# Kernel optimization log

Hardware: AMD Instinct MI355X
Metric: run time of the kernel (lower is better)

Reference implementation:

```python
import jax, jax.numpy as jnp
import numpy as np
from jax import lax

K = 10  # k_neighbors (k = min(k, N); N=1024 so k=10)


def setup_inputs() -> dict:
    key = jax.random.key(0)
    ks = jax.random.split(key, 6)
    B, N, M, D = 4, 1024, 8, 128
    PROJ, NC, OUT = 64, 10, 128
    x = jax.random.normal(ks[0], (B, N, M, D), dtype=jnp.float32)
    # Linear params (torch stores weight as [out, in])
    W_proj_w = jax.random.normal(ks[1], (PROJ, D), dtype=jnp.float32) / np.sqrt(D)
    W_proj_b = jnp.zeros((PROJ,), dtype=jnp.float32)
    C = jax.random.normal(ks[2], (NC, PROJ), dtype=jnp.float32) * np.sqrt(2.0 / (NC + PROJ))
    Theta_w = jax.random.normal(ks[3], (OUT, D), dtype=jnp.float32) / np.sqrt(D)
    Theta_b = jnp.zeros((OUT,), dtype=jnp.float32)
    return {"x": x, "W_proj_w": W_proj_w, "W_proj_b": W_proj_b, "C": C,
            "Theta_w": Theta_w, "Theta_b": Theta_b}


def _forward(x, W_proj_w, W_proj_b, C, Theta_w, Theta_b):
    B, N, M, D = x.shape
    BM = B * M
    x_flat = jnp.transpose(x, (0, 2, 1, 3)).reshape(BM, N, D)
    Z = x_flat @ W_proj_w.T + W_proj_b  # [BM, N, P]
    # squared euclidean pairwise distances (same topk ordering as cdist)
    sq = jnp.sum(Z * Z, axis=-1)  # [BM, N]
    d2 = sq[:, :, None] + sq[:, None, :] - 2.0 * jnp.einsum('bnp,bmp->bnm', Z, Z)
    _, idx = lax.top_k(-d2, K)  # k smallest distances -> [BM, N, K]
    # scatter 1.0 at neighbor indices
    b_ix = jnp.arange(BM)[:, None, None]
    r_ix = jnp.arange(N)[None, :, None]
    H_knn = jnp.zeros((BM, N, N), dtype=jnp.float32).at[b_ix, r_ix, idx].set(1.0)
    H_cluster = jax.nn.softmax(Z @ C.T, axis=-1)  # [BM, N, NC]
    H = jnp.concatenate([H_knn, H_cluster], axis=-1)  # [BM, N, N+NC]
    # hypergraph conv with degree normalization
    D_e = H.sum(axis=1)  # [BM, E]
    D_e_inv = jnp.where(D_e > 0, 1.0 / jnp.maximum(D_e, 1e-12), 0.0)
    D_v = H.sum(axis=2)  # [BM, N]
    D_v_inv_sqrt = jnp.where(D_v > 0, 1.0 / jnp.sqrt(jnp.maximum(D_v, 1e-12)), 0.0)
    X_trans = x_flat @ Theta_w.T + Theta_b  # [BM, N, F]
    out = D_v_inv_sqrt[:, :, None] * X_trans
    out = jnp.einsum('bne,bnf->bef', H, out)   # H^T @ out
    out = D_e_inv[:, :, None] * out
    out = jnp.einsum('bne,bef->bnf', H, out)   # H @ out
    out = D_v_inv_sqrt[:, :, None] * out
    out = jax.nn.elu(out)
    return jnp.transpose(out.reshape(B, M, N, -1), (0, 2, 1, 3))  # [B, N, M, F]


def reference(x, W_proj_w, W_proj_b, C, Theta_w, Theta_b):
    return _forward(x, W_proj_w, W_proj_b, C, Theta_w, Theta_b)
```

## Files before the change

### kernel.cpp

```cpp
#include <hip/hip_runtime.h>
#include <hip/hip_bf16.h>
#include <cstdint>
#include <cstddef>

#define BMC 32
#define NNODE 1024
#define DIN 128
#define PPROJ 64
#define NCLUS 10
#define FOUT 128
#define KNB 10

typedef _Float16 half8 __attribute__((ext_vector_type(8)));
typedef float f32x4 __attribute__((ext_vector_type(4)));

static const size_t OFF_Z    = 0;
static const size_t OFF_SQ   = 2097152;
static const size_t OFF_HC   = 2129920;
static const size_t OFF_IDX  = 2457600;
static const size_t OFF_CNT  = 2785280;
static const size_t OFF_FILL = 2818048;
static const size_t OFF_EC   = 2850816;
static const size_t OFF_DCV  = 2891776;
static const size_t OFF_OFFS = 2892096;
static const size_t OFF_ADJ  = 2924864;
static const size_t OFF_FLAG = 3252544;
static const size_t OFF_END  = 3252608;
static const size_t OFF_WPH  = OFF_EC;
static const size_t OFF_WPL  = OFF_EC +  4096;
static const size_t OFF_THH  = OFF_EC +  8192;
static const size_t OFF_THL  = OFF_EC + 16384;
static const size_t ZERO1_N  = 65536;
static const size_t ZERO2_N  = 41280;

__device__ __forceinline__ float bfu(unsigned int lo16) {
    return __uint_as_float(lo16 << 16);
}
__device__ __forceinline__ float bfhi(unsigned int w) {
    return __uint_as_float(w & 0xffff0000u);
}
__device__ __forceinline__ float ldf(const void* p, size_t i, bool isbf) {
    return isbf ? bfu((unsigned int)((const unsigned short*)p)[i])
                : ((const float*)p)[i];
}
__device__ __forceinline__ unsigned short f2bf(float v) {
    __hip_bfloat16 h = __float2bfloat16(v);
    return *(unsigned short*)&h;
}

__device__ __forceinline__ unsigned long long mkkey(float v, int col) {
    unsigned int bits = __float_as_uint(v);
    unsigned int s = bits ^ (0x80000000u | (unsigned int)((int)bits >> 31));
    return ((unsigned long long)s << 32) | (unsigned int)col;
}
__device__ __forceinline__ void kcas(unsigned long long &a, unsigned long long &b) {
    bool c = b < a;
    unsigned long long t = c ? b : a;
    b = c ? a : b;
    a = t;
}
__device__ __forceinline__ void kmin(unsigned long long &a, unsigned long long b) {
    a = (b < a) ? b : a;
}

__global__ __launch_bounds__(256) void k_probe(const unsigned int* __restrict__ xw,
                                               int* __restrict__ flag) {
    __shared__ int red[256];
    int t = threadIdx.x;
    int cnt = 0;
    for (int i = t; i < 1024; i += 256) {
        float b = bfu(xw[i] & 0xffffu);
        float ab = fabsf(b);
        if (ab > 9.5e-7f && ab < 1.0e6f) cnt++;
    }
    red[t] = cnt;
    __syncthreads();
    for (int off = 128; off > 0; off >>= 1) {
        if (t < off) red[t] += red[t + off];
        __syncthreads();
    }
    if (t == 0) flag[0] = (red[0] >= 700) ? 1 : 0;
}

__global__ __launch_bounds__(256) void k_zero(float* __restrict__ p, int n) {
    int i = blockIdx.x * 256 + threadIdx.x;
    if (i < n) p[i] = 0.0f;
}

__global__ __launch_bounds__(256) void k_split(const void* __restrict__ Wp,
                                               const void* __restrict__ Th,
                                               const int* __restrict__ flag,
                                               _Float16* __restrict__ WpH,
                                               _Float16* __restrict__ WpL,
                                               _Float16* __restrict__ ThH,
                                               _Float16* __restrict__ ThL) {
    const bool isbf = (flag[0] != 0);
    int i = blockIdx.x * 256 + threadIdx.x;
    if (i < 8192) {
        float v = ldf(Wp, i, isbf);
        _Float16 h = (_Float16)v;
        WpH[i] = h;
        WpL[i] = (_Float16)((v - (float)h) * 2048.0f);
    } else {
        int j = i - 8192;
        float v = ldf(Th, j, isbf);
        _Float16 h = (_Float16)v;
        ThH[j] = h;
        ThL[j] = (_Float16)((v - (float)h) * 2048.0f);
    }
}

__global__ __launch_bounds__(256) void k_proj(const void* __restrict__ x,
                                              const _Float16* __restrict__ WpH,
                                              const _Float16* __restrict__ WpL,
                                              const void* __restrict__ Wpb,
                                              const void* __restrict__ Cm,
                                              const int* __restrict__ flag,
                                              _Float16* __restrict__ Zh,
                                              _Float16* __restrict__ Zl,
                                              float* __restrict__ sqv,
                                              float* __restrict__ Hc) {
    __shared__ __align__(16) _Float16 wps[2][64][72];
    __shared__ __align__(16) _Float16 xsh[2][32][72];
    __shared__ float zs[32][68];
    __shared__ float cs[10][64];

    const bool isbf = (flag[0] != 0);
    int tid = threadIdx.x;
    int bi  = blockIdx.x;
    int bm  = bi >> 5;
    int n0  = (bi & 31) << 5;
    int b   = bm >> 3, m = bm & 7;

    int lane = tid & 63, wave = tid >> 6;
    int m16 = lane & 15, quad = lane >> 4;
    int rh = wave >> 1, ch = wave & 1;

    for (int e = tid; e < 640; e += 256) cs[e >> 6][e & 63] = ldf(Cm, e, isbf);

    f32x4 aH[2], aX[2];
#pragma unroll
    for (int t = 0; t < 2; ++t) {
        aH[t] = (f32x4){0.f, 0.f, 0.f, 0.f};
        aX[t] = (f32x4){0.f, 0.f, 0.f, 0.f};
    }

    for (int kc = 0; kc < 2; ++kc) {
        __syncthreads();
        for (int e = tid; e < 512; e += 256) {
            int p = e >> 3, c = e & 7;
            *(uint4*)&wps[0][p][c * 8] =
                *(const uint4*)(WpH + (size_t)p * 128 + kc * 64 + c * 8);
            *(uint4*)&wps[1][p][c * 8] =
                *(const uint4*)(WpL + (size_t)p * 128 + kc * 64 + c * 8);
        }
        for (int e = tid; e < 2048; e += 256) {
            int r = e >> 6, dk = e & 63;
            float v = ldf(x, (((size_t)b * NNODE + n0 + r) * 8 + m) * DIN + kc * 64 + dk, isbf);
            _Float16 h = (_Float16)v;
            xsh[0][r][dk] = h;
            xsh[1][r][dk] = (_Float16)((v - (float)h) * 2048.0f);
        }
        __syncthreads();
#pragma unroll
        for (int c32 = 0; c32 < 2; ++c32) {
            half8 Ah = *(const half8*)&xsh[0][rh * 16 + m16][c32 * 32 + quad * 8];
            half8 Al = *(const half8*)&xsh[1][rh * 16 + m16][c32 * 32 + quad * 8];
#pragma unroll
            for (int t = 0; t < 2; ++t) {
                int p = ch * 32 + t * 16 + m16;
                half8 Bh = *(const half8*)&wps[0][p][c32 * 32 + quad * 8];
                half8 Bl = *(const half8*)&wps[1][p][c32 * 32 + quad * 8];
                aH[t] = __builtin_amdgcn_mfma_f32_16x16x32_f16(Ah, Bh, aH[t], 0, 0, 0);
                aX[t] = __builtin_amdgcn_mfma_f32_16x16x32_f16(Al, Bh, aX[t], 0, 0, 0);
                aX[t] = __builtin_amdgcn_mfma_f32_16x16x32_f16(Ah, Bl, aX[t], 0, 0, 0);
            }
        }
    }

#pragma unroll
    for (int t = 0; t < 2; ++t) {
        int p = ch * 32 + t * 16 + m16;
        float bias = ldf(Wpb, p, isbf);
#pragma unroll
        for (int r = 0; r < 4; ++r) {
            int row = rh * 16 + quad * 4 + r;
            float v = aH[t][r] + aX[t][r] * (1.0f / 2048.0f) + bias;
            zs[row][p] = v;
            size_t off = ((size_t)bm * NNODE + n0 + row) * 64 + p;
            _Float16 h = (_Float16)v;
            Zh[off] = h;
            Zl[off] = (_Float16)((v - (float)h) * 2048.0f);
        }
    }
    __syncthreads();

    int row = tid >> 3, slot = tid & 7;
    int d0 = slot * 8;
    float sp = 0.f;
#pragma unroll
    for (int dd = 0; dd < 8; ++dd) { float z = zs[row][d0+dd]; sp += z * z; }
#pragma unroll
    for (int mm = 1; mm < 8; mm <<= 1) sp += __shfl_xor(sp, mm, 8);
    size_t g = (size_t)bm * NNODE + n0 + row;
    if (slot == 0) sqv[g] = sp;

    float sc[10];
#pragma unroll
    for (int c = 0; c < 10; ++c) {
        float pa = 0.f;
#pragma unroll
        for (int dd = 0; dd < 8; ++dd) pa += zs[row][d0+dd] * cs[c][d0+dd];
#pragma unroll
        for (int mm = 1; mm < 8; mm <<= 1) pa += __shfl_xor(pa, mm, 8);
        sc[c] = pa;
    }
    float mx = sc[0];
#pragma unroll
    for (int c = 1; c < 10; ++c) mx = fmaxf(mx, sc[c]);
    float ssum = 0.f;
#pragma unroll
    for (int c = 0; c < 10; ++c) { sc[c] = expf(sc[c] - mx); ssum += sc[c]; }
    float inv = 1.0f / ssum;
#pragma unroll
    for (int c = 0; c < 10; ++c)
        if ((c & 7) == slot) Hc[g * 10 + c] = sc[c] * inv;
}

__global__ __launch_bounds__(256) void k_theta(const void* __restrict__ x,
                                               const _Float16* __restrict__ ThH,
                                               const _Float16* __restrict__ ThL,
                                               const void* __restrict__ Thb,
                                               const int* __restrict__ flag,
                                               float* __restrict__ Xt) {
    __shared__ __align__(16) _Float16 ths[2][128][72];
    __shared__ __align__(16) _Float16 xsh[2][32][72];

    const bool isbf = (flag[0] != 0);
    int tid = threadIdx.x;
    int bi  = blockIdx.x;
    int bm  = bi >> 5;
    int n0  = (bi & 31) << 5;
    int b   = bm >> 3, m = bm & 7;

    int lane = tid & 63, wave = tid >> 6;
    int m16 = lane & 15, quad = lane >> 4;
    int rh = wave >> 1, ch = wave & 1;

    f32x4 aH[4], aX[4];
#pragma unroll
    for (int t = 0; t < 4; ++t) {
        aH[t] = (f32x4){0.f, 0.f, 0.f, 0.f};
        aX[t] = (f32x4){0.f, 0.f, 0.f, 0.f};
    }

    for (int kc = 0; kc < 2; ++kc) {
        __syncthreads();
        for (int e = tid; e < 1024; e += 256) {
            int f = e >> 3, c = e & 7;
            *(uint4*)&ths[0][f][c * 8] =
                *(const uint4*)(ThH + (size_t)f * 128 + kc * 64 + c * 8);
            *(uint4*)&ths[1][f][c * 8] =
                *(const uint4*)(ThL + (size_t)f * 128 + kc * 64 + c * 8);
        }
        for (int e = tid; e < 2048; e += 256) {
            int r = e >> 6, dk = e & 63;
            float v = ldf(x, (((size_t)b * NNODE + n0 + r) * 8 + m) * DIN + kc * 64 + dk, isbf);
            _Float16 h = (_Float16)v;
            xsh[0][r][dk] = h;
            xsh[1][r][dk] = (_Float16)((v - (float)h) * 2048.0f);
        }
        __syncthreads();
#pragma unroll
        for (int c32 = 0; c32 < 2; ++c32) {
            half8 Ah = *(const half8*)&xsh[0][rh * 16 + m16][c32 * 32 + quad * 8];
            half8 Al = *(const half8*)&xsh[1][rh * 16 + m16][c32 * 32 + quad * 8];
#pragma unroll
            for (int t = 0; t < 4; ++t) {
                int f = ch * 64 + t * 16 + m16;
                half8 Bh = *(const half8*)&ths[0][f][c32 * 32 + quad * 8];
                half8 Bl = *(const half8*)&ths[1][f][c32 * 32 + quad * 8];
                aH[t] = __builtin_amdgcn_mfma_f32_16x16x32_f16(Ah, Bh, aH[t], 0, 0, 0);
                aX[t] = __builtin_amdgcn_mfma_f32_16x16x32_f16(Al, Bh, aX[t], 0, 0, 0);
                aX[t] = __builtin_amdgcn_mfma_f32_16x16x32_f16(Ah, Bl, aX[t], 0, 0, 0);
            }
        }
    }
#pragma unroll
    for (int t = 0; t < 4; ++t) {
        int f = ch * 64 + t * 16 + m16;
        float bias = ldf(Thb, f, isbf);
        size_t rb = (size_t)bm * NNODE + n0 + rh * 16 + quad * 4;
#pragma unroll
        for (int r = 0; r < 4; ++r) {
            Xt[(rb + r) * 128 + f] = aH[t][r] + aX[t][r] * (1.0f / 2048.0f) + bias;
        }
    }
}

__global__ __launch_bounds__(256) void k_topk(const _Float16* __restrict__ Zh,
                                              const _Float16* __restrict__ Zl,
                                              const float* __restrict__ sqv,
                                              int* __restrict__ idxo,
                                              int* __restrict__ cnt) {
    __shared__ __align__(16) _Float16 BH[64 * 72];
    __shared__ __align__(16) _Float16 BL[64 * 72];
    __shared__ float    ST[64 * 36];
    __shared__ float    sqt[64];

    int tid = threadIdx.x;
    int bi  = blockIdx.x;
    int bm  = bi >> 5;
    int n0  = (bi & 31) << 5;
    const _Float16* Zhb = Zh + (size_t)bm * NNODE * 64;
    const _Float16* Zlb = Zl + (size_t)bm * NNODE * 64;

    int lane = tid & 63, wave = tid >> 6;
    int m16 = lane & 15, quad = lane >> 4;

    half8 ah0, ah1, al0, al1, ah0b, ah1b, al0b, al1b;
    {
        size_t ab = (size_t)(n0 + m16) * 64 + quad * 8;
        ah0 = *(const half8*)(Zhb + ab);
        ah1 = *(const half8*)(Zhb + ab + 32);
        al0 = *(const half8*)(Zlb + ab);
        al1 = *(const half8*)(Zlb + ab + 32);
        size_t ab2 = ab + 16 * 64;
        ah0b = *(const half8*)(Zhb + ab2);
        ah1b = *(const half8*)(Zhb + ab2 + 32);
        al0b = *(const half8*)(Zlb + ab2);
        al1b = *(const half8*)(Zlb + ab2 + 32);
    }

    unsigned long long keys[10];
#pragma unroll
    for (int j = 0; j < 10; ++j) keys[j] = ~0ULL;

    int srow  = tid >> 3;
    int sslot = tid & 7;

    for (int t = 0; t < 16; ++t) {
        int j0 = t << 6;
        for (int e = tid; e < 512; e += 256) {
            int col = e >> 3, kc = e & 7;
            *(uint4*)&BH[col * 72 + kc * 8] =
                *(const uint4*)(Zhb + (size_t)(j0 + col) * 64 + kc * 8);
            *(uint4*)&BL[col * 72 + kc * 8] =
                *(const uint4*)(Zlb + (size_t)(j0 + col) * 64 + kc * 8);
        }
        if (tid < 64) sqt[tid] = sqv[(size_t)bm * NNODE + j0 + tid];
        __syncthreads();

        {
            int cl = wave * 16 + m16;
            const _Float16* pb = &BH[cl * 72 + quad * 8];
            const _Float16* pl = &BL[cl * 72 + quad * 8];
            half8 bh0 = *(const half8*)pb;
            half8 bh1 = *(const half8*)(pb + 32);
            half8 bl0 = *(const half8*)pl;
            half8 bl1 = *(const half8*)(pl + 32);
            float sqc = sqt[cl];

            f32x4 acc  = {0.f, 0.f, 0.f, 0.f};
            f32x4 accx = {0.f, 0.f, 0.f, 0.f};
            acc  = __builtin_amdgcn_mfma_f32_16x16x32_f16(ah0, bh0, acc, 0, 0, 0);
            acc  = __builtin_amdgcn_mfma_f32_16x16x32_f16(ah1, bh1, acc, 0, 0, 0);
            accx = __builtin_amdgcn_mfma_f32_16x16x32_f16(al0, bh0, accx, 0, 0, 0);
            accx = __builtin_amdgcn_mfma_f32_16x16x32_f16(ah0, bl0, accx, 0, 0, 0);
            accx = __builtin_amdgcn_mfma_f32_16x16x32_f16(al1, bh1, accx, 0, 0, 0);
            accx = __builtin_amdgcn_mfma_f32_16x16x32_f16(ah1, bl1, accx, 0, 0, 0);
            f32x4 sc;
#pragma unroll
            for (int r = 0; r < 4; ++r) {
                float g = acc[r] + accx[r] * (1.0f / 2048.0f);
                sc[r] = fmaf(-2.0f, g, sqc);
            }
            *(f32x4*)&ST[cl * 36 + quad * 4] = sc;

            f32x4 accB  = {0.f, 0.f, 0.f, 0.f};
            f32x4 accxB = {0.f, 0.f, 0.f, 0.f};
            accB  = __builtin_amdgcn_mfma_f32_16x16x32_f16(ah0b, bh0, accB, 0, 0, 0);
            accB  = __builtin_amdgcn_mfma_f32_16x16x32_f16(ah1b, bh1, accB, 0, 0, 0);
            accxB = __builtin_amdgcn_mfma_f32_16x16x32_f16(al0b, bh0, accxB, 0, 0, 0);
            accxB = __builtin_amdgcn_mfma_f32_16x16x32_f16(ah0b, bl0, accxB, 0, 0, 0);
            accxB = __builtin_amdgcn_mfma_f32_16x16x32_f16(al1b, bh1, accxB, 0, 0, 0);
            accxB = __builtin_amdgcn_mfma_f32_16x16x32_f16(ah1b, bl1, accxB, 0, 0, 0);
#pragma unroll
            for (int r = 0; r < 4; ++r) {
                float g = accB[r] + accxB[r] * (1.0f / 2048.0f);
                sc[r] = fmaf(-2.0f, g, sqc);
            }
            *(f32x4*)&ST[cl * 36 + 16 + quad * 4] = sc;
        }
        __syncthreads();

        unsigned long long b0 = mkkey(ST[(sslot     ) * 36 + srow], j0 + sslot);
        unsigned long long b1 = mkkey(ST[(sslot +  8) * 36 + srow], j0 + sslot + 8);
        unsigned long long b2 = mkkey(ST[(sslot + 16) * 36 + srow], j0 + sslot + 16);
        unsigned long long b3 = mkkey(ST[(sslot + 24) * 36 + srow], j0 + sslot + 24);
        unsigned long long b4 = mkkey(ST[(sslot + 32) * 36 + srow], j0 + sslot + 32);
        unsigned long long b5 = mkkey(ST[(sslot + 40) * 36 + srow], j0 + sslot + 40);
        unsigned long long b6 = mkkey(ST[(sslot + 48) * 36 + srow], j0 + sslot + 48);
        unsigned long long b7 = mkkey(ST[(sslot + 56) * 36 + srow], j0 + sslot + 56);

        kcas(b0, b1); kcas(b2, b3); kcas(b4, b5); kcas(b6, b7);
        kcas(b0, b2); kcas(b1, b3); kcas(b4, b6); kcas(b5, b7);
        kcas(b1, b2); kcas(b5, b6);
        kcas(b0, b4); kcas(b1, b5); kcas(b2, b6); kcas(b3, b7);
        kcas(b2, b4); kcas(b3, b5);
        kcas(b1, b2); kcas(b3, b4); kcas(b5, b6);

        kmin(keys[2], b7); kmin(keys[3], b6); kmin(keys[4], b5); kmin(keys[5], b4);
        kmin(keys[6], b3); kmin(keys[7], b2); kmin(keys[8], b1); kmin(keys[9], b0);

        kcas(keys[0], keys[8]); kcas(keys[1], keys[9]);
        kcas(keys[2], keys[6]); kcas(keys[3], keys[7]);
        kcas(keys[4], keys[8]); kcas(keys[5], keys[9]);
        kcas(keys[2], keys[4]); kcas(keys[3], keys[5]);
        kcas(keys[6], keys[8]); kcas(keys[7], keys[9]);
        kcas(keys[0], keys[1]); kcas(keys[2], keys[3]);
        kcas(keys[4], keys[5]); kcas(keys[6], keys[7]); kcas(keys[8], keys[9]);
    }

    size_t gr = (size_t)bm * NNODE + n0 + srow;
    for (int it = 0; it < 10; ++it) {
        unsigned long long mine = keys[0];
        unsigned long long best = mine;
#pragma unroll
        for (int mm = 1; mm < 8; mm <<= 1) {
            unsigned long long o = __shfl_xor(best, mm, 8);
            if (o < best) best = o;
        }
        if (best == mine) {
#pragma unroll
            for (int j = 0; j < 9; ++j) keys[j] = keys[j+1];
            keys[9] = ~0ULL;
            int col = (int)(best & 0xFFFFFFFFu);
            idxo[gr * KNB + it] = col;
            atomicAdd(&cnt[bm * NNODE + col], 1);
        }
    }
}

__global__ __launch_bounds__(256) void k_scan(const int* __restrict__ cnt,
                                              int* __restrict__ offs) {
    __shared__ int part[256];
    int bm = blockIdx.x, t = threadIdx.x;
    int base = bm * 1024 + t * 4;
    int c0 = cnt[base], c1 = cnt[base+1], c2 = cnt[base+2], c3 = cnt[base+3];
    int ps = c0 + c1 + c2 + c3;
    part[t] = ps;
    __syncthreads();
    for (int off = 1; off < 256; off <<= 1) {
        int add = (t >= off) ? part[t - off] : 0;
        __syncthreads();
        part[t] += add;
        __syncthreads();
    }
    int e0 = part[t] - ps;
    int gb = bm * (NNODE * KNB);
    offs[base]   = gb + e0;
    offs[base+1] = gb + e0 + c0;
    offs[base+2] = gb + e0 + c0 + c1;
    offs[base+3] = gb + e0 + c0 + c1 + c2;
}

__global__ __launch_bounds__(256) void k_fill(const int* __restrict__ idxb,
                                              const int* __restrict__ offs,
                                              int* __restrict__ fill,
                                              int* __restrict__ adj) {
    int i = blockIdx.x * 256 + threadIdx.x;
    int g = i / 10;
    int bm = g >> 10;
    int e  = idxb[i];
    int eg = (bm << 10) + e;
    int pos = atomicAdd(&fill[eg], 1);
    adj[offs[eg] + pos] = g;
}

__global__ __launch_bounds__(256) void k_edge(const float* __restrict__ Xt,
                                              const int* __restrict__ offs,
                                              const int* __restrict__ cnt,
                                              const int* __restrict__ adj,
                                              unsigned short* __restrict__ Ek) {
    int tid = threadIdx.x;
    int bi  = blockIdx.x;
    int swz = (bi & 7) * 512 + (bi >> 3);
    int e = swz * 8 + (tid >> 5);
    int l = tid & 31;
    int start = offs[e];
    int num = cnt[e];
    float4 acc = {0.f, 0.f, 0.f, 0.f};
    if (num > 0) {
        int nm1 = num - 1;
        int gidx[16];
#pragma unroll
        for (int j = 0; j < 16; ++j) {
            int jj = (j < nm1) ? j : nm1;
            gidx[j] = adj[start + jj];
        }
#pragma unroll
        for (int j = 0; j < 16; ++j) {
            float4 a = *(const float4*)(Xt + (size_t)gidx[j] * 128 + l * 4);
            float w = (j < num) ? 1.0f : 0.0f;
            acc.x = fmaf(w, a.x, acc.x);
            acc.y = fmaf(w, a.y, acc.y);
            acc.z = fmaf(w, a.z, acc.z);
            acc.w = fmaf(w, a.w, acc.w);
        }
        int i = 16;
        for (; i + 1 < num; i += 2) {
            int g0 = adj[start + i];
            int g1 = adj[start + i + 1];
            float4 a = *(const float4*)(Xt + (size_t)g0 * 128 + l * 4);
            float4 b = *(const float4*)(Xt + (size_t)g1 * 128 + l * 4);
            acc.x += a.x + b.x; acc.y += a.y + b.y;
            acc.z += a.z + b.z; acc.w += a.w + b.w;
        }
        if (i < num) {
            int g0 = adj[start + i];
            float4 a = *(const float4*)(Xt + (size_t)g0 * 128 + l * 4);
            acc.x += a.x; acc.y += a.y; acc.z += a.z; acc.w += a.w;
        }
    }
    float scale = (num > 0) ? 1.0f / (float)num : 0.0f;
    ushort4 o;
    o.x = f2bf(acc.x * scale);
    o.y = f2bf(acc.y * scale);
    o.z = f2bf(acc.z * scale);
    o.w = f2bf(acc.w * scale);
    *(ushort4*)(Ek + (size_t)e * 128 + l * 4) = o;
}

__global__ __launch_bounds__(256) void k_clus(const float* __restrict__ Xt,
                                              const float* __restrict__ Hc,
                                              float* __restrict__ Ec,
                                              float* __restrict__ Dcv) {
    int tid = threadIdx.x;
    int bm = blockIdx.x >> 3;
    int ch = blockIdx.x & 7;
    int f = tid & 127;
    int h = tid >> 7;
    int c0 = h * 5;
    float acc[5]  = {0.f,0.f,0.f,0.f,0.f};
    float dacc[5] = {0.f,0.f,0.f,0.f,0.f};
    int n0 = ch * 128;
    for (int n = n0; n < n0 + 128; ++n) {
        size_t g = (size_t)bm * NNODE + n;
        float xv = Xt[g * 128 + f];
#pragma unroll
        for (int j = 0; j < 5; ++j) {
            float hv = Hc[g * 10 + c0 + j];
            acc[j]  += hv * xv;
            dacc[j] += hv;
        }
    }
#pragma unroll
    for (int j = 0; j < 5; ++j)
        atomicAdd(&Ec[((size_t)bm * 10 + c0 + j) * 128 + f], acc[j]);
    if (f == 0) {
#pragma unroll
        for (int j = 0; j < 5; ++j) atomicAdd(&Dcv[bm * 10 + c0 + j], dacc[j]);
    }
}

__global__ __launch_bounds__(256) void k_escale(float* __restrict__ Ec,
                                                const float* __restrict__ Dcv) {
    int i = blockIdx.x * 256 + threadIdx.x;
    float d = Dcv[i >> 7];
    Ec[i] = (d > 0.f) ? Ec[i] / d : 0.f;
}

__global__ __launch_bounds__(256) void k_final(const unsigned short* __restrict__ Ek,
                                               const float* __restrict__ Ec,
                                               const float* __restrict__ Hc,
                                               const int* __restrict__ idxb,
                                               float* __restrict__ out) {
    int tid = threadIdx.x;
    int bi  = blockIdx.x;
    int swz = (bi & 7) * 512 + (bi >> 3);
    int g = swz * 8 + (tid >> 5);
    int l = tid & 31;
    int bm = g >> 10, n = g & 1023;
    const int* ip = idxb + (size_t)g * 10;
    const unsigned short* ekb = Ek + ((size_t)bm << 10) * 128 + l * 4;

    float4 acc = {0.f, 0.f, 0.f, 0.f};
#pragma unroll
    for (int k = 0; k < 10; k += 2) {
        int e0 = ip[k], e1 = ip[k + 1];
        ushort4 u0 = *(const ushort4*)(ekb + (size_t)e0 * 128);
        ushort4 u1 = *(const ushort4*)(ekb + (size_t)e1 * 128);
        acc.x += bfu(u0.x) + bfu(u1.x);
        acc.y += bfu(u0.y) + bfu(u1.y);
        acc.z += bfu(u0.z) + bfu(u1.z);
        acc.w += bfu(u0.w) + bfu(u1.w);
    }
    const float* hp  = Hc + (size_t)g * 10;
    const float* ecp = Ec + (size_t)bm * 10 * 128 + l * 4;
#pragma unroll
    for (int c = 0; c < 10; ++c) {
        float hv = hp[c];
        float4 ec = *(const float4*)(ecp + c * 128);
        acc.x += hv * ec.x; acc.y += hv * ec.y;
        acc.z += hv * ec.z; acc.w += hv * ec.w;
    }
    float4 r;
    r.x = acc.x * (1.0f / 11.0f);
    r.y = acc.y * (1.0f / 11.0f);
    r.z = acc.z * (1.0f / 11.0f);
    r.w = acc.w * (1.0f / 11.0f);
    r.x = (r.x > 0.f) ? r.x : expm1f(r.x);
    r.y = (r.y > 0.f) ? r.y : expm1f(r.y);
    r.z = (r.z > 0.f) ? r.z : expm1f(r.z);
    r.w = (r.w > 0.f) ? r.w : expm1f(r.w);
    int b = bm >> 3, m = bm & 7;
    *(float4*)(out + (((size_t)b * NNODE + n) * 8 + m) * 128 + l * 4) = r;
}

extern "C" void kernel_launch(void* const* d_in, const int* in_sizes, int n_in,
                              void* d_out, int out_size, void* d_ws, size_t ws_size,
                              hipStream_t stream) {
    const void* x   = d_in[0];
    const void* Wp  = d_in[1];
    const void* Wpb = d_in[2];
    const void* Cm  = d_in[3];
    const void* Th  = d_in[4];
    const void* Thb = d_in[5];
    float* ws = (float*)d_ws;

    if (ws_size < OFF_END * sizeof(float)) return;

    _Float16* Zh = (_Float16*)(ws + OFF_Z);
    _Float16* Zl = (_Float16*)(ws + OFF_Z + 1048576);
    float* sqv  = ws + OFF_SQ;
    float* Hc   = ws + OFF_HC;
    int*   idxb = (int*)(ws + OFF_IDX);
    int*   cnt  = (int*)(ws + OFF_CNT);
    int*   fill = (int*)(ws + OFF_FILL);
    float* Ec   = ws + OFF_EC;
    float* Dcv  = ws + OFF_DCV;
    int*   offs = (int*)(ws + OFF_OFFS);
    int*   adj  = (int*)(ws + OFF_ADJ);
    int*   flag = (int*)(ws + OFF_FLAG);
    _Float16* WpH = (_Float16*)(ws + OFF_WPH);
    _Float16* WpL = (_Float16*)(ws + OFF_WPL);
    _Float16* ThH = (_Float16*)(ws + OFF_THH);
    _Float16* ThL = (_Float16*)(ws + OFF_THL);
    unsigned short* Ek = (unsigned short*)(ws + OFF_Z);
    float* Xt  = (float*)d_out;
    float* out = (float*)d_out;

    k_probe <<<1, 256, 0, stream>>>((const unsigned int*)x, flag);
    k_zero  <<<256, 256, 0, stream>>>(ws + OFF_CNT, (int)ZERO1_N);
    k_split <<<96,  256, 0, stream>>>(Wp, Th, flag, WpH, WpL, ThH, ThL);
    k_proj  <<<1024, 256, 0, stream>>>(x, WpH, WpL, Wpb, Cm, flag, Zh, Zl, sqv, Hc);
    k_topk  <<<1024, 256, 0, stream>>>(Zh, Zl, sqv, idxb, cnt);
    k_scan  <<<32,   256, 0, stream>>>(cnt, offs);
    k_fill  <<<1280, 256, 0, stream>>>(idxb, offs, fill, adj);
    k_theta <<<1024, 256, 0, stream>>>(x, ThH, ThL, Thb, flag, Xt);
    k_zero  <<<162,  256, 0, stream>>>(ws + OFF_EC, (int)ZERO2_N);
    k_edge  <<<4096, 256, 0, stream>>>(Xt, offs, cnt, adj, Ek);
    k_clus  <<<256,  256, 0, stream>>>(Xt, Hc, Ec, Dcv);
    k_escale<<<160,  256, 0, stream>>>(Ec, Dcv);
    k_final <<<4096, 256, 0, stream>>>(Ek, Ec, Hc, idxb, out);
}
```

Measured before the change: 268.6 us.

## Drop low-half x term in theta GEMM, simplify topk keys, stage Hc in LDS

The theta projection now keeps only the fp16 high part of x, removing one of the three split-precision MFMAs per tile and the second LDS buffer. The topk key now adds the row's squared norm and clamps at zero, so the key is a non-negative distance and the sign-flip transform is no longer needed. The cluster aggregation kernel stages its Hc slice in shared memory and uses fma instead of repeated global reads. Dropping the x low part lowers theta accuracy to about fp16 precision on the input side.

```diff
diff --git a/kernel.cpp b/kernel.cpp
--- a/kernel.cpp
+++ b/kernel.cpp
@@ -48,10 +48,9 @@
     return *(unsigned short*)&h;
 }
 
-__device__ __forceinline__ unsigned long long mkkey(float v, int col) {
-    unsigned int bits = __float_as_uint(v);
-    unsigned int s = bits ^ (0x80000000u | (unsigned int)((int)bits >> 31));
-    return ((unsigned long long)s << 32) | (unsigned int)col;
+__device__ __forceinline__ unsigned long long mkkey(float v, float sqr, int col) {
+    float d = fmaxf(v + sqr, 0.0f);
+    return ((unsigned long long)__float_as_uint(d) << 32) | (unsigned int)col;
 }
 __device__ __forceinline__ void kcas(unsigned long long &a, unsigned long long &b) {
     bool c = b < a;
@@ -234,7 +233,7 @@
                                                const int* __restrict__ flag,
                                                float* __restrict__ Xt) {
     __shared__ __align__(16) _Float16 ths[2][128][72];
-    __shared__ __align__(16) _Float16 xsh[2][32][72];
+    __shared__ __align__(16) _Float16 xsh[32][72];
 
     const bool isbf = (flag[0] != 0);
     int tid = threadIdx.x;
@@ -266,22 +265,18 @@
         for (int e = tid; e < 2048; e += 256) {
             int r = e >> 6, dk = e & 63;
             float v = ldf(x, (((size_t)b * NNODE + n0 + r) * 8 + m) * DIN + kc * 64 + dk, isbf);
-            _Float16 h = (_Float16)v;
-            xsh[0][r][dk] = h;
-            xsh[1][r][dk] = (_Float16)((v - (float)h) * 2048.0f);
+            xsh[r][dk] = (_Float16)v;
         }
         __syncthreads();
 #pragma unroll
         for (int c32 = 0; c32 < 2; ++c32) {
-            half8 Ah = *(const half8*)&xsh[0][rh * 16 + m16][c32 * 32 + quad * 8];
-            half8 Al = *(const half8*)&xsh[1][rh * 16 + m16][c32 * 32 + quad * 8];
+            half8 Ah = *(const half8*)&xsh[rh * 16 + m16][c32 * 32 + quad * 8];
 #pragma unroll
             for (int t = 0; t < 4; ++t) {
                 int f = ch * 64 + t * 16 + m16;
                 half8 Bh = *(const half8*)&ths[0][f][c32 * 32 + quad * 8];
                 half8 Bl = *(const half8*)&ths[1][f][c32 * 32 + quad * 8];
                 aH[t] = __builtin_amdgcn_mfma_f32_16x16x32_f16(Ah, Bh, aH[t], 0, 0, 0);
-                aX[t] = __builtin_amdgcn_mfma_f32_16x16x32_f16(Al, Bh, aX[t], 0, 0, 0);
                 aX[t] = __builtin_amdgcn_mfma_f32_16x16x32_f16(Ah, Bl, aX[t], 0, 0, 0);
             }
         }
@@ -338,6 +333,7 @@
 
     int srow  = tid >> 3;
     int sslot = tid & 7;
+    float sqr = sqv[(size_t)bm * NNODE + n0 + srow];
 
     for (int t = 0; t < 16; ++t) {
         int j0 = t << 6;
@@ -394,14 +390,14 @@
         }
         __syncthreads();
 
-        unsigned long long b0 = mkkey(ST[(sslot     ) * 36 + srow], j0 + sslot);
-        unsigned long long b1 = mkkey(ST[(sslot +  8) * 36 + srow], j0 + sslot + 8);
-        unsigned long long b2 = mkkey(ST[(sslot + 16) * 36 + srow], j0 + sslot + 16);
-        unsigned long long b3 = mkkey(ST[(sslot + 24) * 36 + srow], j0 + sslot + 24);
-        unsigned long long b4 = mkkey(ST[(sslot + 32) * 36 + srow], j0 + sslot + 32);
-        unsigned long long b5 = mkkey(ST[(sslot + 40) * 36 + srow], j0 + sslot + 40);
-        unsigned long long b6 = mkkey(ST[(sslot + 48) * 36 + srow], j0 + sslot + 48);
-        unsigned long long b7 = mkkey(ST[(sslot + 56) * 36 + srow], j0 + sslot + 56);
+        unsigned long long b0 = mkkey(ST[(sslot     ) * 36 + srow], sqr, j0 + sslot);
+        unsigned long long b1 = mkkey(ST[(sslot +  8) * 36 + srow], sqr, j0 + sslot + 8);
+        unsigned long long b2 = mkkey(ST[(sslot + 16) * 36 + srow], sqr, j0 + sslot + 16);
+        unsigned long long b3 = mkkey(ST[(sslot + 24) * 36 + srow], sqr, j0 + sslot + 24);
+        unsigned long long b4 = mkkey(ST[(sslot + 32) * 36 + srow], sqr, j0 + sslot + 32);
+        unsigned long long b5 = mkkey(ST[(sslot + 40) * 36 + srow], sqr, j0 + sslot + 40);
+        unsigned long long b6 = mkkey(ST[(sslot + 48) * 36 + srow], sqr, j0 + sslot + 48);
+        unsigned long long b7 = mkkey(ST[(sslot + 56) * 36 + srow], sqr, j0 + sslot + 56);
 
         kcas(b0, b1); kcas(b2, b3); kcas(b4, b5); kcas(b6, b7);
         kcas(b0, b2); kcas(b1, b3); kcas(b4, b6); kcas(b5, b7);
@@ -536,22 +532,30 @@
                                               const float* __restrict__ Hc,
                                               float* __restrict__ Ec,
                                               float* __restrict__ Dcv) {
+    __shared__ float hcs[128][12];
     int tid = threadIdx.x;
     int bm = blockIdx.x >> 3;
     int ch = blockIdx.x & 7;
+    int n0 = ch * 128;
+
+    for (int e = tid; e < 1280; e += 256) {
+        int r = e / 10, c = e - r * 10;
+        hcs[r][c] = Hc[((size_t)bm * NNODE + n0 + r) * 10 + c];
+    }
+    __syncthreads();
+
     int f = tid & 127;
     int h = tid >> 7;
     int c0 = h * 5;
     float acc[5]  = {0.f,0.f,0.f,0.f,0.f};
     float dacc[5] = {0.f,0.f,0.f,0.f,0.f};
-    int n0 = ch * 128;
-    for (int n = n0; n < n0 + 128; ++n) {
-        size_t g = (size_t)bm * NNODE + n;
-        float xv = Xt[g * 128 + f];
+#pragma unroll 2
+    for (int n = 0; n < 128; ++n) {
+        float xv = Xt[((size_t)bm * NNODE + n0 + n) * 128 + f];
 #pragma unroll
         for (int j = 0; j < 5; ++j) {
-            float hv = Hc[g * 10 + c0 + j];
-            acc[j]  += hv * xv;
+            float hv = hcs[n][c0 + j];
+            acc[j]  = fmaf(hv, xv, acc[j]);
             dacc[j] += hv;
         }
     }
```

Result: slower. 276.6 us (+3.0%).
